# Performance work log

Hardware: AMD Instinct MI355X
Metric: run time of the kernel (lower is better)

The kernel has to match this reference:

```python
import jax, jax.numpy as jnp
import numpy as np

B, T, E, H = 2, 2048, 1024, 16
D = E // H
K_KEEP = 391
RECENCY = 64
SCALE = D ** -0.5


def setup_inputs() -> dict:
    key = jax.random.key(0)
    k1, k2, k3 = jax.random.split(key, 3)
    x = jax.random.normal(k1, (B, T, E), jnp.float32)
    W_attn = jax.random.normal(k2, (3 * E, E), jnp.float32) * 0.02  # torch Linear weight [out,in]
    W_proj = jax.random.normal(k3, (E, E), jnp.float32) * 0.02
    return {"x": x, "W_attn": W_attn, "W_proj": W_proj}


def reference(x, W_attn, W_proj):
    b, t, c = x.shape
    qkv = x @ W_attn.T                      # [B,T,3E]
    q, k, v = jnp.split(qkv, 3, axis=-1)
    to_heads = lambda u: u.reshape(b, t, H, D).transpose(0, 2, 1, 3)  # [B,H,T,D]
    q, k, v = to_heads(q), to_heads(k), to_heads(v)

    # first pass: causal attention weights for importance scoring
    scores = jnp.einsum('bhqd,bhkd->bhqk', q, k) * SCALE
    causal = jnp.tril(jnp.ones((t, t), dtype=bool))
    scores = jnp.where(causal, scores, -jnp.inf)
    attn_w = jax.nn.softmax(scores, axis=-1)

    # mean importance over query dim, force-keep recent tokens
    imp = attn_w.mean(axis=2)               # [B,H,T]
    imp = imp.at[:, :, -RECENCY:].set(1.0)

    # top-k token selection per (batch, head)
    _, idx = jax.lax.top_k(imp, K_KEEP)     # [B,H,K]

    # gather pruned K/V
    K_keep = jnp.take_along_axis(k, idx[..., None], axis=2)  # [B,H,K,D]
    V_keep = jnp.take_along_axis(v, idx[..., None], axis=2)

    # second attention pass over pruned keys (no causal mask, matches legacy code)
    s2 = jnp.einsum('bhqd,bhkd->bhqk', q, K_keep) * SCALE
    a2 = jax.nn.softmax(s2, axis=-1)
    out = jnp.einsum('bhqk,bhkd->bhqd', a2, V_keep)          # [B,H,T,D]

    out = out.transpose(0, 2, 1, 3).reshape(b, t, c)
    return out @ W_proj.T
```

## Files before the change

### kernel.cpp

```cpp
#include <hip/hip_runtime.h>
#include <hip/hip_bf16.h>


#define TT 2048
#define EE 1024
#define HH 16
#define DD 64
#define KKEEP 391
#define REC 64
#define NBH 32
#define QSCALE 0.125f
#define KPAD 448

typedef short bf16x8 __attribute__((ext_vector_type(8)));
typedef _Float16 f16x8 __attribute__((ext_vector_type(8)));
typedef float f32x4 __attribute__((ext_vector_type(4)));

static __device__ inline unsigned short bf_rn(float x) {
  unsigned u = __float_as_uint(x);
  unsigned r = u + 0x7fffu + ((u >> 16) & 1u);
  return (unsigned short)(r >> 16);
}
static __device__ inline float bf_up(unsigned short h) {
  return __uint_as_float((unsigned)h << 16);
}
static __device__ inline unsigned pkf16(float a, float b) {
  union { _Float16 h[2]; unsigned u; } t;
  t.h[0] = (_Float16)a; t.h[1] = (_Float16)b; return t.u;
}
static __device__ inline void glds16(const void* g, void* l) {
  __builtin_amdgcn_global_load_lds(
      (const __attribute__((address_space(1))) void*)g,
      (__attribute__((address_space(3))) void*)l, 16, 0, 0);
}

__global__ __launch_bounds__(256) void split_kernel(
    const float* __restrict__ src, unsigned short* __restrict__ ho,
    unsigned short* __restrict__ lo_, int n)
{
  int i = (blockIdx.x * 256 + threadIdx.x) * 4;
  const int stride = gridDim.x * 1024;
  for (; i < n; i += stride) {
    float4 v = *reinterpret_cast<const float4*>(&src[i]);
    ushort4 hh, ll;
    float f;
    hh.x = bf_rn(v.x); f = bf_up(hh.x); ll.x = bf_rn(v.x - f);
    hh.y = bf_rn(v.y); f = bf_up(hh.y); ll.y = bf_rn(v.y - f);
    hh.z = bf_rn(v.z); f = bf_up(hh.z); ll.z = bf_rn(v.z - f);
    hh.w = bf_rn(v.w); f = bf_up(hh.w); ll.w = bf_rn(v.w - f);
    *reinterpret_cast<ushort4*>(&ho[i]) = hh;
    *reinterpret_cast<ushort4*>(&lo_[i]) = ll;
  }
}

__global__ __launch_bounds__(256) void gemm_bf16s_nt(
    const unsigned short* __restrict__ Ah, const unsigned short* __restrict__ Al,
    const unsigned short* __restrict__ Bh, const unsigned short* __restrict__ Bl,
    float* __restrict__ Cc, unsigned short* __restrict__ Qho, unsigned short* __restrict__ Qlo,
    unsigned short* __restrict__ Kho, unsigned short* __restrict__ Klo,
    float* __restrict__ Vo, int M, int N, int Kd, int mode)
{
  __shared__ __align__(16) unsigned short Ahs[128 * 32];
  __shared__ __align__(16) unsigned short Als[128 * 32];
  __shared__ __align__(16) unsigned short Bhs[128 * 32];
  __shared__ __align__(16) unsigned short Bls[128 * 32];
  const int tid = threadIdx.x;
  const int m0 = blockIdx.y * 128, n0 = blockIdx.x * 128;
  const int w = tid >> 6, lane = tid & 63;
  const int wm = w >> 1, wn = w & 1;
  const int l15 = lane & 15, l4 = lane >> 4;

  size_t gA[2], gB[2]; int ldso[2];
#pragma unroll
  for (int s = 0; s < 2; s++) {
    int seg = w * 2 + s;
    int r = seg * 16 + (lane >> 2);
    int kb = (lane & 3) ^ ((r >> 1) & 3);
    gA[s] = (size_t)(m0 + r) * Kd + kb * 8;
    gB[s] = (size_t)(n0 + r) * Kd + kb * 8;
    ldso[s] = seg * 512;
  }

  f32x4 acc[4][4] = {};

  for (int k0 = 0; k0 < Kd; k0 += 32) {
#pragma unroll
    for (int s = 0; s < 2; s++) {
      glds16(&Ah[gA[s] + k0], &Ahs[ldso[s]]);
      glds16(&Al[gA[s] + k0], &Als[ldso[s]]);
      glds16(&Bh[gB[s] + k0], &Bhs[ldso[s]]);
      glds16(&Bl[gB[s] + k0], &Bls[ldso[s]]);
    }
    __syncthreads();
    bf16x8 ah[4], al[4], bh[4], bl[4];
#pragma unroll
    for (int i = 0; i < 4; i++) {
      int ar = wm * 64 + i * 16 + l15;
      int aoff = ar * 32 + ((l4 ^ ((ar >> 1) & 3)) * 8);
      ah[i] = *reinterpret_cast<const bf16x8*>(&Ahs[aoff]);
      al[i] = *reinterpret_cast<const bf16x8*>(&Als[aoff]);
      int br = wn * 64 + i * 16 + l15;
      int boff = br * 32 + ((l4 ^ ((br >> 1) & 3)) * 8);
      bh[i] = *reinterpret_cast<const bf16x8*>(&Bhs[boff]);
      bl[i] = *reinterpret_cast<const bf16x8*>(&Bls[boff]);
    }
#pragma unroll
    for (int i = 0; i < 4; i++)
#pragma unroll
      for (int j = 0; j < 4; j++) {
        acc[i][j] = __builtin_amdgcn_mfma_f32_16x16x32_bf16(ah[i], bh[j], acc[i][j], 0, 0, 0);
        acc[i][j] = __builtin_amdgcn_mfma_f32_16x16x32_bf16(ah[i], bl[j], acc[i][j], 0, 0, 0);
        acc[i][j] = __builtin_amdgcn_mfma_f32_16x16x32_bf16(al[i], bh[j], acc[i][j], 0, 0, 0);
      }
    __syncthreads();
  }

  if (mode == 0) {
#pragma unroll
    for (int i = 0; i < 4; i++) {
      int mrow0 = m0 + wm * 64 + i * 16 + l4 * 4;
#pragma unroll
      for (int j = 0; j < 4; j++) {
        int ncol = n0 + wn * 64 + j * 16 + l15;
#pragma unroll
        for (int r = 0; r < 4; r++)
          Cc[(size_t)(mrow0 + r) * N + ncol] = acc[i][j][r];
      }
    }
  } else {
#pragma unroll
    for (int j = 0; j < 4; j++) {
      int n = n0 + wn * 64 + j * 16 + l15;
      int p = n >> 10, rr = n & 1023;
      int h = rr >> 6, d0 = rr & 63;
#pragma unroll
      for (int i = 0; i < 4; i++) {
        int mrow0 = m0 + wm * 64 + i * 16 + l4 * 4;
#pragma unroll
        for (int r = 0; r < 4; r++) {
          int m = mrow0 + r;
          int b = m >> 11, t = m & 2047;
          size_t idx = ((size_t)((b * HH + h) * TT + t)) * DD + d0;
          float v = acc[i][j][r];
          if (p == 2) {
            Vo[idx] = v;
          } else {
            unsigned short hi_ = bf_rn(v);
            unsigned short lo2 = bf_rn(v - bf_up(hi_));
            if (p == 0) { Qho[idx] = hi_; Qlo[idx] = lo2; }
            else        { Kho[idx] = hi_; Klo[idx] = lo2; }
          }
        }
      }
    }
  }
}

__global__ __launch_bounds__(512) void importance3_kernel(
    const unsigned short* __restrict__ Qh, const unsigned short* __restrict__ Ql,
    const unsigned short* __restrict__ Kh, const unsigned short* __restrict__ Kl,
    float* __restrict__ part)
{
  const int pairid = blockIdx.x, bh = blockIdx.y;
  const int tid = threadIdx.x;
  const int w = tid >> 6, lane = tid & 63;
  const int wm = w >> 1, wn = w & 1;
  const int l15 = lane & 15, l4 = lane >> 4;
  __shared__ __align__(16) unsigned short Qhs[128 * 64];
  __shared__ __align__(16) unsigned short Qls[128 * 64];
  __shared__ __align__(16) unsigned short Khs[128 * 64];
  __shared__ __align__(16) unsigned short Kls[128 * 64];
  float* csw = (float*)Khs;
  float* rsb = (float*)Kls;

  int krow[2], kkb[2], klds[2];
#pragma unroll
  for (int s = 0; s < 2; s++) {
    int seg = w * 2 + s;
    int r = seg * 8 + (lane >> 3);
    int k8 = lane & 7;
    krow[s] = r; kkb[s] = k8 ^ (r & 7); klds[s] = seg * 512;
  }

  for (int half = 0; half < 2; half++) {
    const int rt = half ? (15 - pairid) : pairid;
    const int row0 = rt * 128;
    const int nch = rt + 1;
    __syncthreads();
#pragma unroll
    for (int cc = 0; cc < 2; cc++) {
      int c = cc * 512 + tid;
      int r = c >> 3, k8 = c & 7;
      int so = r * 64 + ((k8 ^ (r & 7)) * 8);
      size_t ga = ((size_t)(bh * TT + row0 + r)) * DD + k8 * 8;
      *reinterpret_cast<bf16x8*>(&Qhs[so]) = *reinterpret_cast<const bf16x8*>(&Qh[ga]);
      *reinterpret_cast<bf16x8*>(&Qls[so]) = *reinterpret_cast<const bf16x8*>(&Ql[ga]);
    }

    float rsum[2][4];
#pragma unroll
    for (int i = 0; i < 2; i++)
#pragma unroll
      for (int r = 0; r < 4; r++) rsum[i][r] = 0.f;
    float invl[2][4];

    for (int sweep = 0; sweep < 2; sweep++) {
      for (int ci = 0; ci < nch; ci++) {
        __syncthreads();
#pragma unroll
        for (int s = 0; s < 2; s++) {
          size_t ga = ((size_t)(bh * TT + ci * 128 + krow[s])) * DD + kkb[s] * 8;
          glds16(&Kh[ga], &Khs[klds[s]]);
          glds16(&Kl[ga], &Kls[klds[s]]);
        }
        __syncthreads();
        f32x4 acc[2][4] = {};
#pragma unroll
        for (int ks = 0; ks < 2; ks++) {
          bf16x8 ah[2], al_[2];
#pragma unroll
          for (int i = 0; i < 2; i++) {
            int ar = wm * 32 + i * 16 + l15;
            int off = ar * 64 + (((ks * 4 + l4) ^ (ar & 7)) * 8);
            ah[i]  = *reinterpret_cast<const bf16x8*>(&Qhs[off]);
            al_[i] = *reinterpret_cast<const bf16x8*>(&Qls[off]);
          }
#pragma unroll
          for (int j = 0; j < 4; j++) {
            int br = wn * 64 + j * 16 + l15;
            int off = br * 64 + (((ks * 4 + l4) ^ (br & 7)) * 8);
            bf16x8 bh_ = *reinterpret_cast<const bf16x8*>(&Khs[off]);
            bf16x8 bl_ = *reinterpret_cast<const bf16x8*>(&Kls[off]);
#pragma unroll
            for (int i = 0; i < 2; i++) {
              acc[i][j] = __builtin_amdgcn_mfma_f32_16x16x32_bf16(ah[i], bh_, acc[i][j], 0, 0, 0);
              acc[i][j] = __builtin_amdgcn_mfma_f32_16x16x32_bf16(ah[i], bl_, acc[i][j], 0, 0, 0);
              acc[i][j] = __builtin_amdgcn_mfma_f32_16x16x32_bf16(al_[i], bh_, acc[i][j], 0, 0, 0);
            }
          }
        }
        const bool diag = (ci == rt);
        if (sweep == 0) {
#pragma unroll
          for (int i = 0; i < 2; i++)
#pragma unroll
            for (int r = 0; r < 4; r++) {
              int row = row0 + wm * 32 + i * 16 + l4 * 4 + r;
              float s = 0.f;
#pragma unroll
              for (int j = 0; j < 4; j++) {
                int key = ci * 128 + wn * 64 + j * 16 + l15;
                float p = __expf(acc[i][j][r] * QSCALE);
                if (diag && key > row) p = 0.f;
                s += p;
              }
              rsum[i][r] += s;
            }
        } else {
          float cp[4];
#pragma unroll
          for (int j = 0; j < 4; j++) cp[j] = 0.f;
#pragma unroll
          for (int i = 0; i < 2; i++)
#pragma unroll
            for (int r = 0; r < 4; r++) {
              int row = row0 + wm * 32 + i * 16 + l4 * 4 + r;
              float il = invl[i][r];
#pragma unroll
              for (int j = 0; j < 4; j++) {
                int key = ci * 128 + wn * 64 + j * 16 + l15;
                float p = __expf(acc[i][j][r] * QSCALE) * il;
                if (diag && key > row) p = 0.f;
                cp[j] += p;
              }
            }
#pragma unroll
          for (int j = 0; j < 4; j++) {
            float v = cp[j];
            v += __shfl_xor(v, 16); v += __shfl_xor(v, 32);
            cp[j] = v;
          }
          __syncthreads();
          if (l4 == 0) {
#pragma unroll
            for (int j = 0; j < 4; j++)
              csw[w * 128 + wn * 64 + j * 16 + l15] = cp[j];
          }
          __syncthreads();
          if (tid < 128) {
            int wnc = tid >> 6;
            float s = csw[(0 * 2 + wnc) * 128 + tid] + csw[(1 * 2 + wnc) * 128 + tid] +
                      csw[(2 * 2 + wnc) * 128 + tid] + csw[(3 * 2 + wnc) * 128 + tid];
            size_t pi = ((size_t)(bh * 8 + pairid)) * 2048 + ci * 128 + tid;
            bool wr = (half == 0) || (ci > pairid);
            part[pi] = wr ? s : (part[pi] + s);
          }
        }
      }
      if (sweep == 0) {
#pragma unroll
        for (int i = 0; i < 2; i++)
#pragma unroll
          for (int r = 0; r < 4; r++) {
            float v = rsum[i][r];
            v += __shfl_xor(v, 1); v += __shfl_xor(v, 2);
            v += __shfl_xor(v, 4); v += __shfl_xor(v, 8);
            rsum[i][r] = v;
          }
        __syncthreads();
        if (l15 == 0) {
#pragma unroll
          for (int i = 0; i < 2; i++)
#pragma unroll
            for (int r = 0; r < 4; r++)
              rsb[wn * 128 + wm * 32 + i * 16 + l4 * 4 + r] = rsum[i][r];
        }
        __syncthreads();
#pragma unroll
        for (int i = 0; i < 2; i++)
#pragma unroll
          for (int r = 0; r < 4; r++) {
            int rl = wm * 32 + i * 16 + l4 * 4 + r;
            invl[i][r] = 1.0f / (rsb[rl] + rsb[128 + rl]);
          }
      }
    }
  }
}

__global__ __launch_bounds__(256) void topk_gather_kernel(
    const float* __restrict__ part,
    const unsigned short* __restrict__ Kh, const unsigned short* __restrict__ Kl,
    const float* __restrict__ V,
    unsigned short* __restrict__ Kf, unsigned short* __restrict__ Vt)
{
  const int bh = blockIdx.x, tid = threadIdx.x;
  const int lane = tid & 63, w = tid >> 6;
  __shared__ int redi[4];
  __shared__ int stot;
  __shared__ int base[256];
  __shared__ int idxb[KKEEP];
  unsigned u[8];
#pragma unroll
  for (int k = 0; k < 8; k++) {
    int e = tid * 8 + k;
    float s = 0.f;
#pragma unroll
    for (int p = 0; p < 8; p++)
      if (e < (16 - p) * 128) s += part[((size_t)(bh * 8 + p)) * 2048 + e];
    float v = (e >= TT - REC) ? 3.0e3f : s;
    u[k] = __float_as_uint(v);
  }
  unsigned lo = 0u, hi = 0x7f800000u;
  for (int it = 0; it < 31; it++) {
    unsigned mid = lo + ((hi - lo + 1) >> 1);
    int c = 0;
#pragma unroll
    for (int k = 0; k < 8; k++) c += (u[k] >= mid) ? 1 : 0;
#pragma unroll
    for (int off = 1; off <= 32; off <<= 1) c += __shfl_xor(c, off);
    if (lane == 0) redi[w] = c;
    __syncthreads();
    int tot = redi[0] + redi[1] + redi[2] + redi[3];
    if (tot >= KKEEP) lo = mid; else hi = mid - 1;
    __syncthreads();
  }
  const unsigned vstar = lo;
  int cgt = 0, ceq = 0;
#pragma unroll
  for (int k = 0; k < 8; k++) { cgt += (u[k] > vstar) ? 1 : 0; ceq += (u[k] == vstar) ? 1 : 0; }
  base[tid] = cgt; __syncthreads();
  if (tid == 0) {
    int run = 0;
    for (int i = 0; i < 256; i++) { int t = base[i]; base[i] = run; run += t; }
    stot = run;
  }
  __syncthreads();
  int off1 = base[tid];
#pragma unroll
  for (int k = 0; k < 8; k++)
    if (u[k] > vstar) idxb[off1++] = tid * 8 + k;
  __syncthreads();
  base[tid] = ceq; __syncthreads();
  if (tid == 0) {
    int run = 0;
    for (int i = 0; i < 256; i++) { int t = base[i]; base[i] = run; run += t; }
  }
  __syncthreads();
  int off2 = stot + base[tid];
#pragma unroll
  for (int k = 0; k < 8; k++)
    if (u[k] == vstar) { if (off2 < KKEEP) idxb[off2] = tid * 8 + k; off2++; }
  __syncthreads();
  for (int f = tid; f < KPAD * 8; f += 256) {
    int kk = f >> 3, c8 = f & 7;
    union { _Float16 h[8]; uint4 v; } o;
#pragma unroll
    for (int j = 0; j < 8; j++) o.h[j] = (_Float16)0.f;
    if (kk < KKEEP) {
      int sr = idxb[kk];
      bf16x8 hv = *reinterpret_cast<const bf16x8*>(&Kh[((size_t)(bh * TT + sr)) * DD + c8 * 8]);
      bf16x8 lv = *reinterpret_cast<const bf16x8*>(&Kl[((size_t)(bh * TT + sr)) * DD + c8 * 8]);
#pragma unroll
      for (int j = 0; j < 8; j++)
        o.h[j] = (_Float16)(bf_up((unsigned short)hv[j]) + bf_up((unsigned short)lv[j]));
    }
    *reinterpret_cast<uint4*>(&Kf[((size_t)(bh * KPAD) + kk) * DD + c8 * 8]) = o.v;
  }
  for (int f = tid; f < KPAD * 8; f += 256) {
    int kk = f >> 3, d8 = f & 7;
    float vv[8];
#pragma unroll
    for (int j = 0; j < 8; j++) vv[j] = 0.f;
    if (kk < KKEEP) {
      int sr = idxb[kk];
      float4 a = *reinterpret_cast<const float4*>(&V[((size_t)(bh * TT + sr)) * DD + d8 * 8]);
      float4 b = *reinterpret_cast<const float4*>(&V[((size_t)(bh * TT + sr)) * DD + d8 * 8 + 4]);
      vv[0] = a.x; vv[1] = a.y; vv[2] = a.z; vv[3] = a.w;
      vv[4] = b.x; vv[5] = b.y; vv[6] = b.z; vv[7] = b.w;
    }
#pragma unroll
    for (int j = 0; j < 8; j++) {
      union { _Float16 h; unsigned short s; } t;
      t.h = (_Float16)vv[j];
      Vt[((size_t)(bh * DD) + d8 * 8 + j) * KPAD + kk] = t.s;
    }
  }
}

__global__ __launch_bounds__(256) void attn3_kernel(
    const unsigned short* __restrict__ Qh, const unsigned short* __restrict__ Ql,
    const unsigned short* __restrict__ Kf, const unsigned short* __restrict__ Vt,
    unsigned short* __restrict__ AOh, unsigned short* __restrict__ AOl)
{
  const int rt = blockIdx.x, bh = blockIdx.y;
  const int tid = threadIdx.x;
  const int w = tid >> 6, lane = tid & 63;
  const int l15 = lane & 15, l4 = lane >> 4;
  __shared__ __align__(16) unsigned short Qs[64 * 64];
  __shared__ __align__(16) unsigned short Ks[64 * 64];
  __shared__ __align__(16) unsigned short Vs[64 * 64];
  __shared__ float LDSo[4][64][16];
  const int row0 = rt * 64;

#pragma unroll
  for (int it = 0; it < 2; it++) {
    int idx = it * 256 + tid;
    int r = idx >> 3, k8 = idx & 7;
    size_t ga = ((size_t)(bh * TT + row0 + r)) * DD + k8 * 8;
    bf16x8 hv = *reinterpret_cast<const bf16x8*>(&Qh[ga]);
    bf16x8 lv = *reinterpret_cast<const bf16x8*>(&Ql[ga]);
    union { _Float16 h[8]; uint4 v; } q16;
#pragma unroll
    for (int j = 0; j < 8; j++)
      q16.h[j] = (_Float16)(bf_up((unsigned short)hv[j]) + bf_up((unsigned short)lv[j]));
    *reinterpret_cast<uint4*>(&Qs[r * 64 + ((k8 ^ (r & 7)) * 8)]) = q16.v;
  }
  __syncthreads();
  f16x8 bq[2];
#pragma unroll
  for (int ks = 0; ks < 2; ks++) {
    int br = w * 16 + l15;
    bq[ks] = *reinterpret_cast<const f16x8*>(&Qs[br * 64 + (((ks * 4 + l4) ^ (br & 7)) * 8)]);
  }

  int srow[2], skb[2], slds[2];
#pragma unroll
  for (int s = 0; s < 2; s++) {
    int seg = w * 2 + s;
    int r = seg * 8 + (lane >> 3);
    int k8 = lane & 7;
    srow[s] = r; skb[s] = k8 ^ (r & 7); slds[s] = seg * 512;
  }

  f32x4 acc_o[4] = {};
  float rsum = 0.f;

  for (int ci = 0; ci < 7; ci++) {
    __syncthreads();
#pragma unroll
    for (int s = 0; s < 2; s++) {
      glds16(&Kf[((size_t)(bh * KPAD) + ci * 64 + srow[s]) * DD + skb[s] * 8], &Ks[slds[s]]);
      glds16(&Vt[((size_t)(bh * DD) + srow[s]) * KPAD + ci * 64 + skb[s] * 8], &Vs[slds[s]]);
    }
    __syncthreads();
    f32x4 accs[4] = {};
#pragma unroll
    for (int ks = 0; ks < 2; ks++) {
#pragma unroll
      for (int i = 0; i < 4; i++) {
        int kr = i * 16 + l15;
        f16x8 af = *reinterpret_cast<const f16x8*>(&Ks[kr * 64 + (((ks * 4 + l4) ^ (kr & 7)) * 8)]);
        accs[i] = __builtin_amdgcn_mfma_f32_16x16x32_f16(af, bq[ks], accs[i], 0, 0, 0);
      }
    }
    float p[4][4];
#pragma unroll
    for (int i = 0; i < 4; i++)
#pragma unroll
      for (int r = 0; r < 4; r++) {
        int gk = ci * 64 + i * 16 + l4 * 4 + r;
        float pp = __expf(accs[i][r] * QSCALE);
        if (gk >= KKEEP) pp = 0.f;
        p[i][r] = pp;
        rsum += pp;
      }
    unsigned pkU[4][2];
#pragma unroll
    for (int i = 0; i < 4; i++) {
      pkU[i][0] = pkf16(p[i][0], p[i][1]);
      pkU[i][1] = pkf16(p[i][2], p[i][3]);
    }
#pragma unroll
    for (int ks = 0; ks < 2; ks++) {
      union { f16x8 h; unsigned u[4]; } bp;
#pragma unroll
      for (int wp = 0; wp < 4; wp++) {
        int src = ((l4 & 1) * 2 + (wp >> 1)) * 16 + l15;
        unsigned v0 = (unsigned)__shfl((int)pkU[ks * 2][wp & 1], src);
        unsigned v1 = (unsigned)__shfl((int)pkU[ks * 2 + 1][wp & 1], src);
        bp.u[wp] = (l4 & 2) ? v1 : v0;
      }
#pragma unroll
      for (int i = 0; i < 4; i++) {
        int dr = i * 16 + l15;
        f16x8 av = *reinterpret_cast<const f16x8*>(&Vs[dr * 64 + (((ks * 4 + l4) ^ (dr & 7)) * 8)]);
        acc_o[i] = __builtin_amdgcn_mfma_f32_16x16x32_f16(av, bp.h, acc_o[i], 0, 0, 0);
      }
    }
  }
  rsum += __shfl_xor(rsum, 16);
  rsum += __shfl_xor(rsum, 32);
  float inv = 1.0f / rsum;
#pragma unroll
  for (int i = 0; i < 4; i++)
#pragma unroll
    for (int r = 0; r < 4; r++)
      LDSo[w][i * 16 + l4 * 4 + r][l15] = acc_o[i][r] * inv;
  __syncthreads();
  const int b = bh >> 4, h = bh & 15;
#pragma unroll
  for (int uu = 0; uu < 2; uu++) {
    int u = uu * 64 + lane;
    int q = u >> 3, dc = u & 7;
    int row = row0 + w * 16 + q;
    union { unsigned short s[8]; uint4 v; } sh, sl;
#pragma unroll
    for (int j = 0; j < 8; j++) {
      float v = LDSo[w][dc * 8 + j][q];
      unsigned short hh = bf_rn(v);
      sh.s[j] = hh;
      sl.s[j] = bf_rn(v - bf_up(hh));
    }
    size_t addr = ((size_t)(b * TT + row)) * EE + h * DD + dc * 8;
    *reinterpret_cast<uint4*>(&AOh[addr]) = sh.v;
    *reinterpret_cast<uint4*>(&AOl[addr]) = sl.v;
  }
}

extern "C" void kernel_launch(void* const* d_in, const int* in_sizes, int n_in,
                              void* d_out, int out_size, void* d_ws, size_t ws_size,
                              hipStream_t stream)
{
  const float* x     = (const float*)d_in[0];
  const float* Wattn = (const float*)d_in[1];
  const float* Wproj = (const float*)d_in[2];
  float* out = (float*)d_out;
  float* ws  = (float*)d_ws;

  const size_t SZQ = (size_t)NBH * TT * DD;
  const size_t SZK = (size_t)NBH * KPAD * DD;
  float* Vb   = ws;
  float* part = Vb + SZQ;
  unsigned short* Kf  = (unsigned short*)(part + (size_t)NBH * 8 * TT);
  unsigned short* Vt  = Kf + SZK;
  unsigned short* Qhp = Vt + SZK;
  unsigned short* Qlp = Qhp + SZQ;
  unsigned short* Khp = Qlp + SZQ;
  unsigned short* Klp = Khp + SZQ;
  unsigned short* xh  = Klp + SZQ;
  unsigned short* xl  = xh + (size_t)4096 * 1024;
  unsigned short* Wh  = xl + (size_t)4096 * 1024;
  unsigned short* Wl  = Wh + (size_t)3072 * 1024;
  unsigned short* AOh = xh;
  unsigned short* AOl = xl;
  unsigned short* Ph  = Wh;
  unsigned short* Pl  = Ph + (size_t)1024 * 1024;

  const size_t needB =
      ((size_t)SZQ + (size_t)NBH * 8 * TT) * 4 +
      ((size_t)2 * SZK + (size_t)4 * SZQ + (size_t)2 * 4096 * 1024 + (size_t)2 * 3072 * 1024) * 2;
  if (ws_size < needB) return;

  split_kernel<<<512, 256, 0, stream>>>(x, xh, xl, 4096 * 1024);
  split_kernel<<<512, 256, 0, stream>>>(Wattn, Wh, Wl, 3072 * 1024);
  gemm_bf16s_nt<<<dim3(24, 32), 256, 0, stream>>>(xh, xl, Wh, Wl, nullptr,
                                                  Qhp, Qlp, Khp, Klp, Vb, 4096, 3072, 1024, 1);
  split_kernel<<<512, 256, 0, stream>>>(Wproj, Ph, Pl, 1024 * 1024);
  importance3_kernel<<<dim3(8, NBH), 512, 0, stream>>>(Qhp, Qlp, Khp, Klp, part);
  topk_gather_kernel<<<NBH, 256, 0, stream>>>(part, Khp, Klp, Vb, Kf, Vt);
  attn3_kernel<<<dim3(32, NBH), 256, 0, stream>>>(Qhp, Qlp, Kf, Vt, AOh, AOl);
  gemm_bf16s_nt<<<dim3(8, 32), 256, 0, stream>>>(AOh, AOl, Ph, Pl, out,
                                                 nullptr, nullptr, nullptr, nullptr, nullptr,
                                                 4096, 1024, 1024, 0);
}
```

Baseline: 310.4 us.

## Double-buffer LDS tiles in GEMM and attention kernels, single-product V GEMM

Adds double-buffered shared-memory staging to the QKV/proj GEMM, the importance kernel and the pruned attention kernel. The next tile's global-to-LDS load is issued before the current tile's MFMAs, so load latency overlaps compute, and the barriers are rearranged to fit. Separately, GEMM blocks that produce the V columns skip the low-part loads and the two correction MFMAs, computing V at plain bf16 precision. The attention grids are also transposed so consecutive blocks cover different heads. The cost is twice the LDS per block, which may lower occupancy, plus slightly less accurate V values.

```diff
diff --git a/kernel.cpp b/kernel.cpp
--- a/kernel.cpp
+++ b/kernel.cpp
@@ -60,15 +60,16 @@
     unsigned short* __restrict__ Kho, unsigned short* __restrict__ Klo,
     float* __restrict__ Vo, int M, int N, int Kd, int mode)
 {
-  __shared__ __align__(16) unsigned short Ahs[128 * 32];
-  __shared__ __align__(16) unsigned short Als[128 * 32];
-  __shared__ __align__(16) unsigned short Bhs[128 * 32];
-  __shared__ __align__(16) unsigned short Bls[128 * 32];
+  __shared__ __align__(16) unsigned short Ahs[2][128 * 32];
+  __shared__ __align__(16) unsigned short Als[2][128 * 32];
+  __shared__ __align__(16) unsigned short Bhs[2][128 * 32];
+  __shared__ __align__(16) unsigned short Bls[2][128 * 32];
   const int tid = threadIdx.x;
   const int m0 = blockIdx.y * 128, n0 = blockIdx.x * 128;
   const int w = tid >> 6, lane = tid & 63;
   const int wm = w >> 1, wn = w & 1;
   const int l15 = lane & 15, l4 = lane >> 4;
+  const bool vblk = (mode == 1) && (blockIdx.x >= 16);
 
   size_t gA[2], gB[2]; int ldso[2];
 #pragma unroll
@@ -81,38 +82,51 @@
     ldso[s] = seg * 512;
   }
 
+  auto STAGE = [&](int bb, int k0) {
+#pragma unroll
+    for (int s = 0; s < 2; s++) {
+      glds16(&Ah[gA[s] + k0], &Ahs[bb][ldso[s]]);
+      glds16(&Bh[gB[s] + k0], &Bhs[bb][ldso[s]]);
+      if (!vblk) {
+        glds16(&Al[gA[s] + k0], &Als[bb][ldso[s]]);
+        glds16(&Bl[gB[s] + k0], &Bls[bb][ldso[s]]);
+      }
+    }
+  };
+
   f32x4 acc[4][4] = {};
 
+  STAGE(0, 0);
+  __syncthreads();
+  int cur = 0;
   for (int k0 = 0; k0 < Kd; k0 += 32) {
-#pragma unroll
-    for (int s = 0; s < 2; s++) {
-      glds16(&Ah[gA[s] + k0], &Ahs[ldso[s]]);
-      glds16(&Al[gA[s] + k0], &Als[ldso[s]]);
-      glds16(&Bh[gB[s] + k0], &Bhs[ldso[s]]);
-      glds16(&Bl[gB[s] + k0], &Bls[ldso[s]]);
-    }
-    __syncthreads();
+    if (k0 + 32 < Kd) STAGE(cur ^ 1, k0 + 32);
     bf16x8 ah[4], al[4], bh[4], bl[4];
 #pragma unroll
     for (int i = 0; i < 4; i++) {
       int ar = wm * 64 + i * 16 + l15;
       int aoff = ar * 32 + ((l4 ^ ((ar >> 1) & 3)) * 8);
-      ah[i] = *reinterpret_cast<const bf16x8*>(&Ahs[aoff]);
-      al[i] = *reinterpret_cast<const bf16x8*>(&Als[aoff]);
+      ah[i] = *reinterpret_cast<const bf16x8*>(&Ahs[cur][aoff]);
       int br = wn * 64 + i * 16 + l15;
       int boff = br * 32 + ((l4 ^ ((br >> 1) & 3)) * 8);
-      bh[i] = *reinterpret_cast<const bf16x8*>(&Bhs[boff]);
-      bl[i] = *reinterpret_cast<const bf16x8*>(&Bls[boff]);
+      bh[i] = *reinterpret_cast<const bf16x8*>(&Bhs[cur][boff]);
+      if (!vblk) {
+        al[i] = *reinterpret_cast<const bf16x8*>(&Als[cur][aoff]);
+        bl[i] = *reinterpret_cast<const bf16x8*>(&Bls[cur][boff]);
+      }
     }
 #pragma unroll
     for (int i = 0; i < 4; i++)
 #pragma unroll
       for (int j = 0; j < 4; j++) {
         acc[i][j] = __builtin_amdgcn_mfma_f32_16x16x32_bf16(ah[i], bh[j], acc[i][j], 0, 0, 0);
-        acc[i][j] = __builtin_amdgcn_mfma_f32_16x16x32_bf16(ah[i], bl[j], acc[i][j], 0, 0, 0);
-        acc[i][j] = __builtin_amdgcn_mfma_f32_16x16x32_bf16(al[i], bh[j], acc[i][j], 0, 0, 0);
+        if (!vblk) {
+          acc[i][j] = __builtin_amdgcn_mfma_f32_16x16x32_bf16(ah[i], bl[j], acc[i][j], 0, 0, 0);
+          acc[i][j] = __builtin_amdgcn_mfma_f32_16x16x32_bf16(al[i], bh[j], acc[i][j], 0, 0, 0);
+        }
       }
     __syncthreads();
+    cur ^= 1;
   }
 
   if (mode == 0) {
@@ -161,17 +175,17 @@
     const unsigned short* __restrict__ Kh, const unsigned short* __restrict__ Kl,
     float* __restrict__ part)
 {
-  const int pairid = blockIdx.x, bh = blockIdx.y;
+  const int pairid = blockIdx.y, bh = blockIdx.x;
   const int tid = threadIdx.x;
   const int w = tid >> 6, lane = tid & 63;
   const int wm = w >> 1, wn = w & 1;
   const int l15 = lane & 15, l4 = lane >> 4;
   __shared__ __align__(16) unsigned short Qhs[128 * 64];
   __shared__ __align__(16) unsigned short Qls[128 * 64];
-  __shared__ __align__(16) unsigned short Khs[128 * 64];
-  __shared__ __align__(16) unsigned short Kls[128 * 64];
-  float* csw = (float*)Khs;
-  float* rsb = (float*)Kls;
+  __shared__ __align__(16) unsigned short Khs[2][128 * 64];
+  __shared__ __align__(16) unsigned short Kls[2][128 * 64];
+  __shared__ float csw[8 * 128];
+  __shared__ float rsb[2 * 128];
 
   int krow[2], kkb[2], klds[2];
 #pragma unroll
@@ -181,6 +195,14 @@
     int k8 = lane & 7;
     krow[s] = r; kkb[s] = k8 ^ (r & 7); klds[s] = seg * 512;
   }
+  auto STAGEK = [&](int bb, int ci) {
+#pragma unroll
+    for (int s = 0; s < 2; s++) {
+      size_t ga = ((size_t)(bh * TT + ci * 128 + krow[s])) * DD + kkb[s] * 8;
+      glds16(&Kh[ga], &Khs[bb][klds[s]]);
+      glds16(&Kl[ga], &Kls[bb][klds[s]]);
+    }
+  };
 
   for (int half = 0; half < 2; half++) {
     const int rt = half ? (15 - pairid) : pairid;
@@ -205,15 +227,11 @@
     float invl[2][4];
 
     for (int sweep = 0; sweep < 2; sweep++) {
+      STAGEK(0, 0);
+      __syncthreads();
+      int cur = 0;
       for (int ci = 0; ci < nch; ci++) {
-        __syncthreads();
-#pragma unroll
-        for (int s = 0; s < 2; s++) {
-          size_t ga = ((size_t)(bh * TT + ci * 128 + krow[s])) * DD + kkb[s] * 8;
-          glds16(&Kh[ga], &Khs[klds[s]]);
-          glds16(&Kl[ga], &Kls[klds[s]]);
-        }
-        __syncthreads();
+        if (ci + 1 < nch) STAGEK(cur ^ 1, ci + 1);
         f32x4 acc[2][4] = {};
 #pragma unroll
         for (int ks = 0; ks < 2; ks++) {
@@ -229,8 +247,8 @@
           for (int j = 0; j < 4; j++) {
             int br = wn * 64 + j * 16 + l15;
             int off = br * 64 + (((ks * 4 + l4) ^ (br & 7)) * 8);
-            bf16x8 bh_ = *reinterpret_cast<const bf16x8*>(&Khs[off]);
-            bf16x8 bl_ = *reinterpret_cast<const bf16x8*>(&Kls[off]);
+            bf16x8 bh_ = *reinterpret_cast<const bf16x8*>(&Khs[cur][off]);
+            bf16x8 bl_ = *reinterpret_cast<const bf16x8*>(&Kls[cur][off]);
 #pragma unroll
             for (int i = 0; i < 2; i++) {
               acc[i][j] = __builtin_amdgcn_mfma_f32_16x16x32_bf16(ah[i], bh_, acc[i][j], 0, 0, 0);
@@ -256,6 +274,7 @@
               }
               rsum[i][r] += s;
             }
+          __syncthreads();
         } else {
           float cp[4];
 #pragma unroll
@@ -280,7 +299,6 @@
             v += __shfl_xor(v, 16); v += __shfl_xor(v, 32);
             cp[j] = v;
           }
-          __syncthreads();
           if (l4 == 0) {
 #pragma unroll
             for (int j = 0; j < 4; j++)
@@ -295,7 +313,9 @@
             bool wr = (half == 0) || (ci > pairid);
             part[pi] = wr ? s : (part[pi] + s);
           }
+          __syncthreads();
         }
+        cur ^= 1;
       }
       if (sweep == 0) {
 #pragma unroll
@@ -307,7 +327,6 @@
             v += __shfl_xor(v, 4); v += __shfl_xor(v, 8);
             rsum[i][r] = v;
           }
-        __syncthreads();
         if (l15 == 0) {
 #pragma unroll
           for (int i = 0; i < 2; i++)
@@ -433,15 +452,31 @@
     const unsigned short* __restrict__ Kf, const unsigned short* __restrict__ Vt,
     unsigned short* __restrict__ AOh, unsigned short* __restrict__ AOl)
 {
-  const int rt = blockIdx.x, bh = blockIdx.y;
+  const int rt = blockIdx.y, bh = blockIdx.x;
   const int tid = threadIdx.x;
   const int w = tid >> 6, lane = tid & 63;
   const int l15 = lane & 15, l4 = lane >> 4;
   __shared__ __align__(16) unsigned short Qs[64 * 64];
-  __shared__ __align__(16) unsigned short Ks[64 * 64];
-  __shared__ __align__(16) unsigned short Vs[64 * 64];
+  __shared__ __align__(16) unsigned short Ks[2][64 * 64];
+  __shared__ __align__(16) unsigned short Vs[2][64 * 64];
   __shared__ float LDSo[4][64][16];
   const int row0 = rt * 64;
+
+  int srow[2], skb[2], slds[2];
+#pragma unroll
+  for (int s = 0; s < 2; s++) {
+    int seg = w * 2 + s;
+    int r = seg * 8 + (lane >> 3);
+    int k8 = lane & 7;
+    srow[s] = r; skb[s] = k8 ^ (r & 7); slds[s] = seg * 512;
+  }
+  auto STAGEA = [&](int bb, int ci) {
+#pragma unroll
+    for (int s = 0; s < 2; s++) {
+      glds16(&Kf[((size_t)(bh * KPAD) + ci * 64 + srow[s]) * DD + skb[s] * 8], &Ks[bb][slds[s]]);
+      glds16(&Vt[((size_t)(bh * DD) + srow[s]) * KPAD + ci * 64 + skb[s] * 8], &Vs[bb][slds[s]]);
+    }
+  };
 
 #pragma unroll
   for (int it = 0; it < 2; it++) {
@@ -456,6 +491,7 @@
       q16.h[j] = (_Float16)(bf_up((unsigned short)hv[j]) + bf_up((unsigned short)lv[j]));
     *reinterpret_cast<uint4*>(&Qs[r * 64 + ((k8 ^ (r & 7)) * 8)]) = q16.v;
   }
+  STAGEA(0, 0);
   __syncthreads();
   f16x8 bq[2];
 #pragma unroll
@@ -464,33 +500,19 @@
     bq[ks] = *reinterpret_cast<const f16x8*>(&Qs[br * 64 + (((ks * 4 + l4) ^ (br & 7)) * 8)]);
   }
 
-  int srow[2], skb[2], slds[2];
-#pragma unroll
-  for (int s = 0; s < 2; s++) {
-    int seg = w * 2 + s;
-    int r = seg * 8 + (lane >> 3);
-    int k8 = lane & 7;
-    srow[s] = r; skb[s] = k8 ^ (r & 7); slds[s] = seg * 512;
-  }
-
   f32x4 acc_o[4] = {};
   float rsum = 0.f;
+  int cur = 0;
 
   for (int ci = 0; ci < 7; ci++) {
-    __syncthreads();
-#pragma unroll
-    for (int s = 0; s < 2; s++) {
-      glds16(&Kf[((size_t)(bh * KPAD) + ci * 64 + srow[s]) * DD + skb[s] * 8], &Ks[slds[s]]);
-      glds16(&Vt[((size_t)(bh * DD) + srow[s]) * KPAD + ci * 64 + skb[s] * 8], &Vs[slds[s]]);
-    }
-    __syncthreads();
+    if (ci + 1 < 7) STAGEA(cur ^ 1, ci + 1);
     f32x4 accs[4] = {};
 #pragma unroll
     for (int ks = 0; ks < 2; ks++) {
 #pragma unroll
       for (int i = 0; i < 4; i++) {
         int kr = i * 16 + l15;
-        f16x8 af = *reinterpret_cast<const f16x8*>(&Ks[kr * 64 + (((ks * 4 + l4) ^ (kr & 7)) * 8)]);
+        f16x8 af = *reinterpret_cast<const f16x8*>(&Ks[cur][kr * 64 + (((ks * 4 + l4) ^ (kr & 7)) * 8)]);
         accs[i] = __builtin_amdgcn_mfma_f32_16x16x32_f16(af, bq[ks], accs[i], 0, 0, 0);
       }
     }
@@ -524,10 +546,12 @@
 #pragma unroll
       for (int i = 0; i < 4; i++) {
         int dr = i * 16 + l15;
-        f16x8 av = *reinterpret_cast<const f16x8*>(&Vs[dr * 64 + (((ks * 4 + l4) ^ (dr & 7)) * 8)]);
+        f16x8 av = *reinterpret_cast<const f16x8*>(&Vs[cur][dr * 64 + (((ks * 4 + l4) ^ (dr & 7)) * 8)]);
         acc_o[i] = __builtin_amdgcn_mfma_f32_16x16x32_f16(av, bp.h, acc_o[i], 0, 0, 0);
       }
     }
+    __syncthreads();
+    cur ^= 1;
   }
   rsum += __shfl_xor(rsum, 16);
   rsum += __shfl_xor(rsum, 32);
@@ -597,9 +621,9 @@
   gemm_bf16s_nt<<<dim3(24, 32), 256, 0, stream>>>(xh, xl, Wh, Wl, nullptr,
                                                   Qhp, Qlp, Khp, Klp, Vb, 4096, 3072, 1024, 1);
   split_kernel<<<512, 256, 0, stream>>>(Wproj, Ph, Pl, 1024 * 1024);
-  importance3_kernel<<<dim3(8, NBH), 512, 0, stream>>>(Qhp, Qlp, Khp, Klp, part);
+  importance3_kernel<<<dim3(NBH, 8), 512, 0, stream>>>(Qhp, Qlp, Khp, Klp, part);
   topk_gather_kernel<<<NBH, 256, 0, stream>>>(part, Khp, Klp, Vb, Kf, Vt);
-  attn3_kernel<<<dim3(32, NBH), 256, 0, stream>>>(Qhp, Qlp, Kf, Vt, AOh, AOl);
+  attn3_kernel<<<dim3(NBH, 32), 256, 0, stream>>>(Qhp, Qlp, Kf, Vt, AOh, AOl);
   gemm_bf16s_nt<<<dim3(8, 32), 256, 0, stream>>>(AOh, AOl, Ph, Pl, out,
                                                  nullptr, nullptr, nullptr, nullptr, nullptr,
                                                  4096, 1024, 1024, 0);
```

Result: no change. 313.3 us (+0.9%).
